# Kernel tuning notes

Measured on AMD Instinct MI355X. Metric: run time of the kernel, lower is better.

## Reference

```python
import jax, jax.numpy as jnp
import numpy as np

D = 1024      # input_dim = clip_model.text_projection.shape[1]
P = D // 8    # pre_dim1 == pre_dim2 == 128
B, NS, NT, C = 4096, 8192, 8192, 1000
EPS = 1e-5
SCALE = 0.1
BETA_S = 1.0
BETA_T = 1.0


def setup_inputs() -> dict:
    key = jax.random.key(0)
    ks = jax.random.split(key, 24)
    rn = lambda k, shp, s=0.02: jax.random.normal(k, shp, dtype=jnp.float32) * s
    inp = {
        "Ft": jax.random.normal(ks[0], (C, D), dtype=jnp.float32),
        "Fv": jax.random.normal(ks[1], (B, D), dtype=jnp.float32),
        "Fvs_bank": jax.random.normal(ks[2], (NS, D), dtype=jnp.float32),
        "Fvt_bank": jax.random.normal(ks[3], (NT, D), dtype=jnp.float32),
        # pre_project: Linear(D->P), BN(P), ReLU, Linear(P->P), BN(P), ReLU, Linear(P->3D)
        "W1": rn(ks[4], (P, D)), "b1": jnp.zeros((P,), jnp.float32),
        "g1": jnp.ones((P,), jnp.float32), "be1": jnp.zeros((P,), jnp.float32),
        "m1": jnp.zeros((P,), jnp.float32), "v1": jnp.ones((P,), jnp.float32),
        "W2": rn(ks[5], (P, P)), "b2": jnp.zeros((P,), jnp.float32),
        "g2": jnp.ones((P,), jnp.float32), "be2": jnp.zeros((P,), jnp.float32),
        "m2": jnp.zeros((P,), jnp.float32), "v2": jnp.ones((P,), jnp.float32),
        "W3": rn(ks[6], (3 * D, P)), "b3": jnp.zeros((3 * D,), jnp.float32),
        # post_project: Linear(D->D)
        "Wp": rn(ks[7], (D, D)), "bp": jnp.zeros((D,), jnp.float32),
        "logit_scale": jnp.asarray(np.log(1.0 / 0.07), dtype=jnp.float32),
    }
    return inp


def _pre_project(x, W1, b1, g1, be1, m1, v1, W2, b2, g2, be2, m2, v2, W3, b3):
    # Linear -> BatchNorm1d (eval: running stats) -> ReLU, twice, then Linear to 3*D
    h = x @ W1.T + b1
    h = jax.nn.relu((h - m1) * jax.lax.rsqrt(v1 + EPS) * g1 + be1)
    h = h @ W2.T + b2
    h = jax.nn.relu((h - m2) * jax.lax.rsqrt(v2 + EPS) * g2 + be2)
    return h @ W3.T + b3  # (n, 3*D)


def _qkv(o):
    # einops 'b (d k) -> k b d' with k=3: interleaved split along last dim
    o = o.reshape(o.shape[0], D, 3)
    return o[..., 0], o[..., 1], o[..., 2]


def reference(Ft, Fv, Fvs_bank, Fvt_bank, W1, b1, g1, be1, m1, v1,
              W2, b2, g2, be2, m2, v2, W3, b3, Wp, bp, logit_scale):
    pre = lambda x: _pre_project(x, W1, b1, g1, be1, m1, v1,
                                 W2, b2, g2, be2, m2, v2, W3, b3)
    q_fv, _, _ = _qkv(pre(Fv))
    _, k_fvs, v_fvs = _qkv(pre(Fvs_bank))
    _, k_fvt, v_fvt = _qkv(pre(Fvt_bank))

    As = jax.nn.softmax(SCALE * (q_fv @ k_fvs.T), axis=-1)  # (B, NS)
    At = jax.nn.softmax(SCALE * (q_fv @ k_fvt.T), axis=-1)  # (B, NT)

    Fsa = Fv + (As @ v_fvs) @ Wp.T + bp
    Fta = Fv + (At @ v_fvt) @ Wp.T + bp
    Fsa = Fsa / jnp.linalg.norm(Fsa, axis=-1, keepdims=True)
    Fta = Fta / jnp.linalg.norm(Fta, axis=-1, keepdims=True)

    ls = jnp.exp(logit_scale)
    logits = BETA_S * ls * (Fsa @ Ft.T) + BETA_T * ls * (Fta @ Ft.T)
    return logits  # (B, C)
```

## Files before the change

kernel.cpp:

```cpp
#include <hip/hip_runtime.h>
#include <hip/hip_bf16.h>
#include <math.h>

#define D_DIM   1024
#define P_DIM   128
#define B_ROWS  4096
#define NBANK   8192
#define C_CLS   1000
#define EPS_BN  1e-5f
#define SCALE_S 0.1f
#define MTOT    20480
#define KVSEG   16
#define KCH     64
#define CHUNKS  (NBANK / KVSEG / KCH)

typedef __bf16 bf16x8 __attribute__((ext_vector_type(8)));
typedef float  f32x4  __attribute__((ext_vector_type(4)));
typedef __hip_bfloat16 bf;

__device__ __forceinline__ void load_lds16(const void* gp, void* lp) {
    __builtin_amdgcn_global_load_lds(
        (__attribute__((address_space(1))) void*)gp,
        (__attribute__((address_space(3))) void*)lp, 16, 0, 0);
}

__device__ __forceinline__ int4 pack8(float4 a, float4 b) {
    union { bf h[8]; int4 v; } u;
    u.h[0] = __float2bfloat16(a.x); u.h[1] = __float2bfloat16(a.y);
    u.h[2] = __float2bfloat16(a.z); u.h[3] = __float2bfloat16(a.w);
    u.h[4] = __float2bfloat16(b.x); u.h[5] = __float2bfloat16(b.y);
    u.h[6] = __float2bfloat16(b.z); u.h[7] = __float2bfloat16(b.w);
    return u.v;
}

__global__ __launch_bounds__(256)
void gemm_bf16(const bf* __restrict__ A, const bf* __restrict__ B,
               const bf* __restrict__ B2,
               int M, int N, int K, int lda, int ldb,
               int kchunks, int fx, int fy, int epi,
               float* __restrict__ Cf, bf* __restrict__ Cb,
               const float* __restrict__ bias, const float* __restrict__ biasm,
               const float* __restrict__ bng, const float* __restrict__ bnb,
               const float* __restrict__ bnm, const float* __restrict__ bnv,
               const float* __restrict__ addsrc, const float* __restrict__ lsp,
               int ldc)
{
    __shared__ __align__(16) short ldsS[8192];
    short* lsA = ldsS;
    short* lsB = ldsS + 4096;

    const int tid  = threadIdx.x;
    const int wave = tid >> 6;
    const int lane = tid & 63;
    const int wm   = wave >> 1;
    const int wn   = wave & 1;
    const int r16  = lane & 15;
    const int quad = lane >> 4;

    int bx, by;
    if (fx == 0) {
        bx = blockIdx.x; by = blockIdx.y;
    } else {
        const int gx = gridDim.x, gy = gridDim.y;
        const int l   = blockIdx.y * gx + blockIdx.x;
        const int xcd = l & 7;
        const int i0  = l >> 3;
        const int sx  = gx / fx, sy = gy / fy;
        bx = (xcd % fx) * sx + (i0 % sx);
        by = (xcd / fx) * sy + (i0 / sx);
    }
    const int bm0 = by * 128;
    const int bn0 = bx * 128;
    const bf* Bp = (B2 && by > 0) ? B2 : B;

    const int kper = K / kchunks;
    const int kbeg = blockIdx.z * kper;
    const int kend = kbeg + kper;

    f32x4 acc[4][4];
#pragma unroll
    for (int i = 0; i < 4; ++i)
#pragma unroll
        for (int j = 0; j < 4; ++j) acc[i][j] = (f32x4){0.f, 0.f, 0.f, 0.f};

    for (int k0 = kbeg; k0 < kend; k0 += 32) {
#pragma unroll
        for (int i = 0; i < 2; ++i) {
            const int s   = i * 256 + tid;
            const int row = s >> 2;
            const int cc  = (s & 3) * 8;
            const int lofs = (i * 256 + wave * 64) * 16;
            load_lds16(A + (size_t)(bm0 + row) * lda + k0 + cc, (char*)lsA + lofs);
            load_lds16(Bp + (size_t)(bn0 + row) * ldb + k0 + cc, (char*)lsB + lofs);
        }
        __syncthreads();

        bf16x8 af[4], bfr[4];
#pragma unroll
        for (int i = 0; i < 4; ++i)
            af[i] = *(const bf16x8*)(lsA + (wm * 64 + i * 16 + r16) * 32 + quad * 8);
#pragma unroll
        for (int j = 0; j < 4; ++j)
            bfr[j] = *(const bf16x8*)(lsB + (wn * 64 + j * 16 + r16) * 32 + quad * 8);
#pragma unroll
        for (int i = 0; i < 4; ++i)
#pragma unroll
            for (int j = 0; j < 4; ++j)
                acc[i][j] = __builtin_amdgcn_mfma_f32_16x16x32_bf16(
                    af[i], bfr[j], acc[i][j], 0, 0, 0);
        __syncthreads();
    }

    if (epi == 8) {
        float* dst = Cf + (size_t)blockIdx.z * M * N;
#pragma unroll
        for (int i = 0; i < 4; ++i) {
            const int gmb = bm0 + wm * 64 + i * 16 + quad * 4;
#pragma unroll
            for (int j = 0; j < 4; ++j) {
                const int gn = bn0 + wn * 64 + j * 16 + r16;
#pragma unroll
                for (int r = 0; r < 4; ++r)
                    dst[(size_t)(gmb + r) * N + gn] = acc[i][j][r];
            }
        }
        return;
    }

    if (epi == 3 || epi == 4) {
        const float lsv = (epi == 4) ? expf(*lsp) : 1.0f;
#pragma unroll
        for (int i = 0; i < 4; ++i) {
            const int gmb = bm0 + wm * 64 + i * 16 + quad * 4;
#pragma unroll
            for (int j = 0; j < 4; ++j) {
                const int gn = bn0 + wn * 64 + j * 16 + r16;
#pragma unroll
                for (int r = 0; r < 4; ++r) {
                    const int gm = gmb + r;
                    float val = acc[i][j][r];
                    if (epi == 3) {
                        Cf[(size_t)gm * N + gn] =
                            val + bias[gn] + addsrc[(size_t)(gm & (ldc - 1)) * N + gn];
                    } else {
                        if (gn < ldc) Cf[(size_t)gm * ldc + gn] = val * lsv;
                    }
                }
            }
        }
        return;
    }

    bf* dst = Cb + (epi == 6 ? (size_t)blockIdx.z * M * N : 0);
    bf* my  = (bf*)(ldsS + wave * 2048);

#pragma unroll
    for (int half = 0; half < 2; ++half) {
#pragma unroll
        for (int i2 = 0; i2 < 2; ++i2) {
            const int i = half * 2 + i2;
            const int gmb = bm0 + wm * 64 + i * 16 + quad * 4;
#pragma unroll
            for (int j = 0; j < 4; ++j) {
                const int gn = bn0 + wn * 64 + j * 16 + r16;
#pragma unroll
                for (int r = 0; r < 4; ++r) {
                    float val = acc[i][j][r];
                    if (epi == 1) {
                        val += bias[gn];
                        val = (val - bnm[gn]) * rsqrtf(bnv[gn] + EPS_BN) * bng[gn] + bnb[gn];
                        val = fmaxf(val, 0.f);
                    } else {
                        if (bias)  val += bias[gn];
                        if (biasm) val += biasm[gmb + r];
                    }
                    my[(i2 * 16 + quad * 4 + r) * 64 + j * 16 + r16] =
                        __float2bfloat16(val);
                }
            }
        }
#pragma unroll
        for (int it = 0; it < 4; ++it) {
            const int chunk = it * 64 + lane;
            const int lrow  = chunk >> 3;
            const int lcol  = (chunk & 7) * 8;
            const int grow  = bm0 + wm * 64 + half * 32 + lrow;
            const int gcol  = bn0 + wn * 64 + lcol;
            int4 v = *(const int4*)(my + lrow * 64 + lcol);
            *(int4*)(dst + (size_t)grow * N + gcol) = v;
        }
    }
}

__global__ __launch_bounds__(256)
void h2fuse(const float* __restrict__ Hp,
            const bf* __restrict__ W2b,
            const bf* __restrict__ Wqk,
            const float* __restrict__ bnA,
            const float* __restrict__ vvecP,
            bf* __restrict__ h2b, bf* __restrict__ qtb,
            float* __restrict__ beta, bf* __restrict__ h2T)
{
    __shared__ __align__(16) short lsH[16384];
    __shared__ __align__(16) short lsW[16384];
    __shared__ float sA1[128], sC1[128], sA2[128], sC2[128];

    const int tid  = threadIdx.x;
    const int wave = tid >> 6;
    const int lane = tid & 63;
    const int r16  = lane & 15;
    const int quad = lane >> 4;
    const int wm   = wave >> 1;
    const int wn   = wave & 1;
    const int r0   = blockIdx.x * 128;
    const bool isq = (r0 < B_ROWS);

#pragma unroll
    for (int m = 0; m < 8; ++m) {
        const int s = m * 256 + tid;
        const int row = s >> 4, pcg = s & 15;
        load_lds16(W2b + row * 128 + (pcg ^ (row & 15)) * 8,
                   (char*)lsW + (m * 256 + wave * 64) * 16);
    }
    if (tid < 128) {
        sA1[tid] = bnA[tid];       sC1[tid] = bnA[128 + tid];
        sA2[tid] = bnA[256 + tid]; sC2[tid] = bnA[384 + tid];
    }
    __syncthreads();

#pragma unroll
    for (int m = 0; m < 16; ++m) {
        const int s = m * 256 + tid;
        const int row = s >> 5;
        const int col = (s & 31) * 4;
        const float* p0 = Hp + (size_t)(r0 + row) * 128 + col;
        float4 x0 = *(const float4*)p0;
        float4 x1 = *(const float4*)(p0 + (size_t)MTOT * 128);
        union { bf h[4]; int2 v; } u;
        u.h[0] = __float2bfloat16(fmaxf(fmaf(x0.x + x1.x, sA1[col],     sC1[col]),     0.f));
        u.h[1] = __float2bfloat16(fmaxf(fmaf(x0.y + x1.y, sA1[col + 1], sC1[col + 1]), 0.f));
        u.h[2] = __float2bfloat16(fmaxf(fmaf(x0.z + x1.z, sA1[col + 2], sC1[col + 2]), 0.f));
        u.h[3] = __float2bfloat16(fmaxf(fmaf(x0.w + x1.w, sA1[col + 3], sC1[col + 3]), 0.f));
        const int cg = col >> 3;
        *(int2*)((bf*)lsH + row * 128 + ((cg ^ (row & 15)) << 3) + (col & 7)) = u.v;
    }
    __syncthreads();

    f32x4 acc[4][4];
#pragma unroll
    for (int i = 0; i < 4; ++i)
#pragma unroll
        for (int j = 0; j < 4; ++j) acc[i][j] = (f32x4){0.f, 0.f, 0.f, 0.f};
#pragma unroll
    for (int ks = 0; ks < 4; ++ks) {
        bf16x8 af[4], bfr[4];
#pragma unroll
        for (int i = 0; i < 4; ++i) {
            const int row = wm * 64 + i * 16 + r16;
            af[i] = *(const bf16x8*)(lsH + row * 128 + ((ks * 4 + quad) ^ (row & 15)) * 8);
        }
#pragma unroll
        for (int j = 0; j < 4; ++j) {
            const int row = wn * 64 + j * 16 + r16;
            bfr[j] = *(const bf16x8*)(lsW + row * 128 + ((ks * 4 + quad) ^ (row & 15)) * 8);
        }
#pragma unroll
        for (int i = 0; i < 4; ++i)
#pragma unroll
            for (int j = 0; j < 4; ++j)
                acc[i][j] = __builtin_amdgcn_mfma_f32_16x16x32_bf16(
                    af[i], bfr[j], acc[i][j], 0, 0, 0);
    }
    __syncthreads();

    if (isq) {
#pragma unroll
        for (int m = 0; m < 8; ++m) {
            const int s = m * 256 + tid;
            const int row = s >> 4, pcg = s & 15;
            load_lds16(Wqk + row * 128 + (pcg ^ (row & 15)) * 8,
                       (char*)lsW + (m * 256 + wave * 64) * 16);
        }
    }

#pragma unroll
    for (int i = 0; i < 4; ++i) {
#pragma unroll
        for (int j = 0; j < 4; ++j) {
            const int gn = wn * 64 + j * 16 + r16;
            const int cg = gn >> 3, cl = gn & 7;
            const float a2 = sA2[gn], c2 = sC2[gn];
#pragma unroll
            for (int r = 0; r < 4; ++r) {
                const int row = wm * 64 + i * 16 + quad * 4 + r;
                float v = fmaxf(fmaf(acc[i][j][r], a2, c2), 0.f);
                ((bf*)lsH)[row * 128 + ((cg ^ (row & 15)) << 3) + cl] =
                    __float2bfloat16(v);
            }
        }
    }
    __syncthreads();

    if (!isq) {
#pragma unroll
        for (int m = 0; m < 8; ++m) {
            const int s = m * 256 + tid;
            const int row = s >> 4, cg = s & 15;
            *(int4*)(h2b + (size_t)(r0 + row) * 128 + cg * 8) =
                *(const int4*)(lsH + row * 128 + ((cg ^ (row & 15)) << 3));
        }
        if (tid < 128) {
            float s = 0.f;
#pragma unroll
            for (int z = 0; z < 16; ++z) s += vvecP[z * 128 + tid];
            sA1[tid] = s;
        }
        __syncthreads();
        const int nb0 = r0 - B_ROWS;
        {
            const int row = tid >> 1, hf = tid & 1;
            float s = 0.f;
#pragma unroll
            for (int g = 0; g < 8; ++g) {
                const int cg = hf * 8 + g;
                bf16x8 v = *(const bf16x8*)(lsH + row * 128 + ((cg ^ (row & 15)) << 3));
#pragma unroll
                for (int e = 0; e < 8; ++e)
                    s += __bfloat162float((bf)v[e]) * sA1[cg * 8 + e];
            }
            s += __shfl_xor(s, 1, 64);
            if (hf == 0) beta[nb0 + row] = s;
        }
#pragma unroll
        for (int m = 0; m < 8; ++m) {
            const int idx = m * 256 + tid;
            const int p  = idx >> 4;
            const int ng = (idx & 15) * 8;
            union { bf h[8]; int4 v; } u;
#pragma unroll
            for (int e = 0; e < 8; ++e) {
                const int n = ng + e;
                u.h[e] = ((bf*)lsH)[n * 128 + (((p >> 3) ^ (n & 15)) << 3) + (p & 7)];
            }
            *(int4*)(h2T + (size_t)p * (2 * NBANK) + nb0 + ng) = u.v;
        }
        return;
    }

    f32x4 acc2[4][4];
#pragma unroll
    for (int i = 0; i < 4; ++i)
#pragma unroll
        for (int j = 0; j < 4; ++j) acc2[i][j] = (f32x4){0.f, 0.f, 0.f, 0.f};
#pragma unroll
    for (int ks = 0; ks < 4; ++ks) {
        bf16x8 af[4], bfr[4];
#pragma unroll
        for (int i = 0; i < 4; ++i) {
            const int row = wm * 64 + i * 16 + r16;
            af[i] = *(const bf16x8*)(lsH + row * 128 + ((ks * 4 + quad) ^ (row & 15)) * 8);
        }
#pragma unroll
        for (int j = 0; j < 4; ++j) {
            const int row = wn * 64 + j * 16 + r16;
            bfr[j] = *(const bf16x8*)(lsW + row * 128 + ((ks * 4 + quad) ^ (row & 15)) * 8);
        }
#pragma unroll
        for (int i = 0; i < 4; ++i)
#pragma unroll
            for (int j = 0; j < 4; ++j)
                acc2[i][j] = __builtin_amdgcn_mfma_f32_16x16x32_bf16(
                    af[i], bfr[j], acc2[i][j], 0, 0, 0);
    }
    __syncthreads();

    bf* my  = (bf*)lsW + wave * 2048;
    bf* dst = qtb + (size_t)r0 * 128;
#pragma unroll
    for (int half = 0; half < 2; ++half) {
#pragma unroll
        for (int i2 = 0; i2 < 2; ++i2) {
            const int i = half * 2 + i2;
#pragma unroll
            for (int j = 0; j < 4; ++j)
#pragma unroll
                for (int r = 0; r < 4; ++r)
                    my[(i2 * 16 + quad * 4 + r) * 64 + j * 16 + r16] =
                        __float2bfloat16(acc2[i][j][r]);
        }
#pragma unroll
        for (int it = 0; it < 4; ++it) {
            const int chunk = it * 64 + lane;
            const int lrow  = chunk >> 3;
            const int lcol  = (chunk & 7) * 8;
            const int grow  = wm * 64 + half * 32 + lrow;
            const int gcol  = wn * 64 + lcol;
            int4 v = *(const int4*)(my + lrow * 64 + lcol);
            *(int4*)(dst + (size_t)grow * 128 + gcol) = v;
        }
    }
}

__global__ __launch_bounds__(512)
void attn_fused(const bf* __restrict__ qt,
                const bf* __restrict__ h2bank,
                const bf* __restrict__ h2T,
                const float* __restrict__ beta,
                bf* __restrict__ Ypart,
                float* __restrict__ rsP)
{
    __shared__ __align__(16) short lds[24576];
    short* lsK = lds;
    short* lsV = lds + 8192;
    short* lsS = lds + 16384;

    const int tid  = threadIdx.x;
    const int wave = tid >> 6;
    const int lane = tid & 63;
    const int r16  = lane & 15;
    const int quad = lane >> 4;

    const int qb   = blockIdx.x >> 5;
    const int side = (blockIdx.x >> 4) & 1;
    const int seg  = blockIdx.x & 15;
    const int part = side * KVSEG + seg;
    const int nseg0 = seg * (NBANK / KVSEG);
    const bf* kbase = h2bank + (size_t)side * NBANK * P_DIM;
    const int ncol0 = side * NBANK;

    const bf* qrow = qt + (size_t)(qb * 128 + wave * 16 + r16) * P_DIM;
    bf16x8 qreg[4];
#pragma unroll
    for (int ks = 0; ks < 4; ++ks)
        qreg[ks] = *(const bf16x8*)(qrow + (ks * 4 + quad) * 8);

    f32x4 yacc[8];
    float rsacc[4] = {0.f, 0.f, 0.f, 0.f};
#pragma unroll
    for (int j = 0; j < 8; ++j) yacc[j] = (f32x4){0.f, 0.f, 0.f, 0.f};

    for (int c = 0; c < CHUNKS; ++c) {
        const int kv0 = nseg0 + c * KCH;
        __syncthreads();
#pragma unroll
        for (int m = 0; m < 2; ++m) {
            const int s = m * 512 + tid;
            const int row = s >> 4, pcg = s & 15;
            const int lcg = pcg ^ (row & 15);
            load_lds16(kbase + (size_t)(kv0 + row) * P_DIM + lcg * 8,
                       (char*)lsK + (m * 512 + wave * 64) * 16);
        }
#pragma unroll
        for (int m = 0; m < 2; ++m) {
            const int s = m * 512 + tid;
            const int row = s >> 3, pcg = s & 7;
            const int lcg = pcg ^ (row & 7);
            load_lds16(h2T + (size_t)row * (2 * NBANK) + ncol0 + kv0 + lcg * 8,
                       (char*)lsV + (m * 512 + wave * 64) * 16);
        }
        __syncthreads();

        f32x4 sacc[4];
#pragma unroll
        for (int j = 0; j < 4; ++j) sacc[j] = (f32x4){0.f, 0.f, 0.f, 0.f};
        __builtin_amdgcn_s_setprio(1);
#pragma unroll
        for (int ks = 0; ks < 4; ++ks) {
            bf16x8 bfr[4];
#pragma unroll
            for (int j = 0; j < 4; ++j) {
                const int kr = j * 16 + r16;
                bfr[j] = *(const bf16x8*)(lsK + kr * 128 +
                                          ((ks * 4 + quad) ^ (kr & 15)) * 8);
            }
#pragma unroll
            for (int j = 0; j < 4; ++j)
                sacc[j] = __builtin_amdgcn_mfma_f32_16x16x32_bf16(
                    qreg[ks], bfr[j], sacc[j], 0, 0, 0);
        }
        __builtin_amdgcn_s_setprio(0);

#pragma unroll
        for (int j = 0; j < 4; ++j) {
            const int col = j * 16 + r16;
            const float bv = beta[(size_t)side * NBANK + kv0 + col];
            const int cg = col >> 3, cl = col & 7;
#pragma unroll
            for (int r = 0; r < 4; ++r) {
                const int row = wave * 16 + quad * 4 + r;
                float v = __expf(SCALE_S * (sacc[j][r] + bv));
                rsacc[r] += v;
                ((bf*)lsS)[row * 64 + ((cg ^ (row & 7)) << 3) + cl] =
                    __float2bfloat16(v);
            }
        }

        __builtin_amdgcn_s_setprio(1);
#pragma unroll
        for (int ks = 0; ks < 2; ++ks) {
            const int sr = wave * 16 + r16;
            bf16x8 pa = *(const bf16x8*)(lsS + sr * 64 +
                                         ((ks * 4 + quad) ^ (sr & 7)) * 8);
            bf16x8 pb[8];
#pragma unroll
            for (int j = 0; j < 8; ++j) {
                const int vr = j * 16 + r16;
                pb[j] = *(const bf16x8*)(lsV + vr * 64 +
                                         ((ks * 4 + quad) ^ (vr & 7)) * 8);
            }
#pragma unroll
            for (int j = 0; j < 8; ++j)
                yacc[j] = __builtin_amdgcn_mfma_f32_16x16x32_bf16(
                    pa, pb[j], yacc[j], 0, 0, 0);
        }
        __builtin_amdgcn_s_setprio(0);
    }

#pragma unroll
    for (int r = 0; r < 4; ++r) {
        float s = rsacc[r];
        s += __shfl_xor(s, 1, 64);
        s += __shfl_xor(s, 2, 64);
        s += __shfl_xor(s, 4, 64);
        s += __shfl_xor(s, 8, 64);
        rsacc[r] = s;
    }
    if (r16 == 0)
        *(float4*)(rsP + (size_t)part * B_ROWS + qb * 128 + wave * 16 + quad * 4) =
            (float4){rsacc[0], rsacc[1], rsacc[2], rsacc[3]};

    __syncthreads();
    bf* my = (bf*)lds + wave * 2048;
#pragma unroll
    for (int j = 0; j < 8; ++j)
#pragma unroll
        for (int r = 0; r < 4; ++r)
            my[(quad * 4 + r) * 128 + j * 16 + r16] =
                __float2bfloat16(yacc[j][r]);
    bf* dst = Ypart + (size_t)part * B_ROWS * P_DIM
                    + (size_t)(qb * 128 + wave * 16) * P_DIM;
#pragma unroll
    for (int it = 0; it < 4; ++it) {
        const int chunk = it * 64 + lane;
        const int lrow  = chunk >> 4;
        const int lcol  = (chunk & 15) * 8;
        *(int4*)(dst + (size_t)lrow * P_DIM + lcol) =
            *(const int4*)(my + lrow * 128 + lcol);
    }
}

#define PG0 10240
#define PG1 584
#define PG2 64
#define PG3 512
#define PG4 8
#define PG5 256
#define PG6 1

__global__ __launch_bounds__(256)
void prep(const float* __restrict__ Fv, const float* __restrict__ Fvs,
          const float* __restrict__ Fvt,
          const float* __restrict__ W1, const float* __restrict__ W2,
          const float* __restrict__ Wp,
          const float* __restrict__ W3, const float* __restrict__ b3,
          const float* __restrict__ bp, const float* __restrict__ Ft,
          const float* __restrict__ b1, const float* __restrict__ g1,
          const float* __restrict__ be1, const float* __restrict__ m1,
          const float* __restrict__ v1,
          const float* __restrict__ b2, const float* __restrict__ g2,
          const float* __restrict__ be2, const float* __restrict__ m2,
          const float* __restrict__ v2,
          bf* __restrict__ Xb, bf* __restrict__ W1b, bf* __restrict__ W2b,
          bf* __restrict__ Wpb,
          bf* __restrict__ Tq, bf* __restrict__ Tk, bf* __restrict__ Tv,
          bf* __restrict__ Ftb,
          float* __restrict__ vvecP, float* __restrict__ bvp,
          float* __restrict__ bnA)
{
    const int tid = threadIdx.x;
    int b = blockIdx.x;
    if (b < PG0) {
        int i = (b * 256 + tid) * 8;
        const int n0 = B_ROWS * D_DIM, n1 = n0 + NBANK * D_DIM;
        const float* src; int off;
        if (i < n0)      { src = Fv;  off = i; }
        else if (i < n1) { src = Fvs; off = i - n0; }
        else             { src = Fvt; off = i - n1; }
        float4 a = *(const float4*)(src + off);
        float4 c = *(const float4*)(src + off + 4);
        *(int4*)(Xb + i) = pack8(a, c);
        return;
    }
    if ((b -= PG0) < PG1) {
        int i = (b * 256 + tid) * 8;
        const int n1 = P_DIM * D_DIM, n2 = n1 + P_DIM * P_DIM;
        const float* src; bf* dst; int off;
        if (i < n1)      { src = W1; dst = W1b; off = i; }
        else if (i < n2) { src = W2; dst = W2b; off = i - n1; }
        else             { src = Wp; dst = Wpb; off = i - n2; }
        float4 a = *(const float4*)(src + off);
        float4 c = *(const float4*)(src + off + 4);
        *(int4*)(dst + off) = pack8(a, c);
        return;
    }
    if ((b -= PG1) < PG2) {
        int i = (b * 256 + tid) * 8;
        int p = i >> 10, d0 = i & 1023;
        union { bf h[8]; int4 v; } uq, uk, uv;
#pragma unroll
        for (int j = 0; j < 8; ++j) {
            const float* r = W3 + (size_t)3 * (d0 + j) * P_DIM + p;
            uq.h[j] = __float2bfloat16(r[0]);
            uk.h[j] = __float2bfloat16(r[P_DIM]);
            uv.h[j] = __float2bfloat16(r[2 * P_DIM]);
        }
        *(int4*)(Tq + i) = uq.v;
        *(int4*)(Tk + i) = uk.v;
        *(int4*)(Tv + i) = uv.v;
        return;
    }
    if ((b -= PG2) < PG3) {
        int i = (b * 256 + tid) * 8;
        int row = i >> 10, col = i & 1023;
        if (row < C_CLS) {
            float4 a = *(const float4*)(Ft + (size_t)row * D_DIM + col);
            float4 c = *(const float4*)(Ft + (size_t)row * D_DIM + col + 4);
            *(int4*)(Ftb + i) = pack8(a, c);
        } else {
            *(int4*)(Ftb + i) = (int4){0, 0, 0, 0};
        }
        return;
    }
    if ((b -= PG3) < PG4) {
        const int p = tid & 127, hf = tid >> 7;
        const int dbase = b * 128 + hf * 64;
        float s = 0.f;
        for (int dd = 0; dd < 64; ++dd) {
            const int d = dbase + dd;
            s = fmaf(b3[3 * d], W3[(size_t)(3 * d + 1) * P_DIM + p], s);
        }
        vvecP[(b * 2 + hf) * P_DIM + p] = s;
        return;
    }
    if ((b -= PG4) < PG5) {
        const int wave = tid >> 6, lane = tid & 63;
        const int o = b * 4 + wave;
        const float* r = Wp + (size_t)o * D_DIM;
        float s = 0.f;
        for (int i = lane; i < D_DIM; i += 64) s = fmaf(r[i], b3[3 * i + 2], s);
        for (int off = 32; off > 0; off >>= 1) s += __shfl_down(s, off, 64);
        if (lane == 0) bvp[o] = s + bp[o];
        return;
    }
    if (tid < 128) {
        float a1 = g1[tid] * rsqrtf(v1[tid] + EPS_BN);
        bnA[tid]       = a1;
        bnA[128 + tid] = (b1[tid] - m1[tid]) * a1 + be1[tid];
        float a2 = g2[tid] * rsqrtf(v2[tid] + EPS_BN);
        bnA[256 + tid] = a2;
        bnA[384 + tid] = (b2[tid] - m2[tid]) * a2 + be2[tid];
    }
}

__global__ __launch_bounds__(256)
void reduceWW(const bf* __restrict__ WWp,
              bf* __restrict__ Wqk, bf* __restrict__ Wpv)
{
    const int tid = threadIdx.x;
    const size_t pstride = (size_t)1152 * 128;
    if (blockIdx.x < 8) {
        int i = (blockIdx.x * 256 + tid) * 8;
        float s[8] = {};
        for (int z = 0; z < 8; ++z) {
            union { int4 v; bf h[8]; } u;
            u.v = *(const int4*)(WWp + (size_t)z * pstride + i);
#pragma unroll
            for (int e = 0; e < 8; ++e) s[e] += __bfloat162float(u.h[e]);
        }
        union { bf h[8]; int4 v; } o;
#pragma unroll
        for (int e = 0; e < 8; ++e) o.h[e] = __float2bfloat16(s[e]);
        *(int4*)(Wqk + i) = o.v;
    } else {
        int i = ((blockIdx.x - 8) * 256 + tid) * 8;
        float s[8] = {};
        for (int z = 0; z < 8; ++z) {
            union { int4 v; bf h[8]; } u;
            u.v = *(const int4*)(WWp + (size_t)z * pstride + 16384 + i);
#pragma unroll
            for (int e = 0; e < 8; ++e) s[e] += __bfloat162float(u.h[e]);
        }
        union { bf h[8]; int4 v; } o;
#pragma unroll
        for (int e = 0; e < 8; ++e) o.h[e] = __float2bfloat16(s[e]);
        *(int4*)(Wpv + i) = o.v;
    }
}

__global__ __launch_bounds__(256)
void reduceY(const bf* __restrict__ parts, const float* __restrict__ rsP,
             bf* __restrict__ Yhat)
{
    int j = (blockIdx.x * 256 + threadIdx.x) * 8;
    const int s = j >> 19;
    const int qrow = (j >> 7) & (B_ROWS - 1);
    float rs = 0.f;
#pragma unroll
    for (int g = 0; g < KVSEG; ++g)
        rs += rsP[(size_t)(s * KVSEG + g) * B_ROWS + qrow];
    const bf* p = parts + (size_t)s * KVSEG * 524288 + (size_t)(j & 524287);
    float acc[8] = {};
    for (int z = 0; z < KVSEG; ++z) {
        union { int4 v; bf h[8]; } u;
        u.v = *(const int4*)(p + (size_t)z * 524288);
#pragma unroll
        for (int e = 0; e < 8; ++e) acc[e] += __bfloat162float(u.h[e]);
    }
    const float inv = 1.0f / rs;
    union { bf h[8]; int4 v; } o;
#pragma unroll
    for (int e = 0; e < 8; ++e) o.h[e] = __float2bfloat16(acc[e] * inv);
    *(int4*)(Yhat + j) = o.v;
}

__global__ __launch_bounds__(256)
void rownorm2b(const float* __restrict__ G, bf* __restrict__ out)
{
    __shared__ float red[16];
    const int tid = threadIdx.x;
    const float* ps = G + (size_t)blockIdx.x * D_DIM;
    const float* pt = ps + (size_t)B_ROWS * D_DIM;
    float4 a = *(const float4*)(ps + tid * 4);
    float4 c = *(const float4*)(pt + tid * 4);
    float sa = a.x * a.x + a.y * a.y + a.z * a.z + a.w * a.w;
    float sb = c.x * c.x + c.y * c.y + c.z * c.z + c.w * c.w;
    for (int s = 32; s > 0; s >>= 1) {
        sa += __shfl_down(sa, s, 64);
        sb += __shfl_down(sb, s, 64);
    }
    if ((tid & 63) == 0) { red[tid >> 6] = sa; red[8 + (tid >> 6)] = sb; }
    __syncthreads();
    if (tid == 0) {
        float ta = 0.f, tb = 0.f;
        for (int w = 0; w < 4; ++w) { ta += red[w]; tb += red[8 + w]; }
        red[4] = rsqrtf(ta); red[12] = rsqrtf(tb);
    }
    __syncthreads();
    const float ia = red[4], ib = red[12];
    union { bf h[4]; int2 v; } o;
    o.h[0] = __float2bfloat16(a.x * ia + c.x * ib);
    o.h[1] = __float2bfloat16(a.y * ia + c.y * ib);
    o.h[2] = __float2bfloat16(a.z * ia + c.z * ib);
    o.h[3] = __float2bfloat16(a.w * ia + c.w * ib);
    *(int2*)(out + (size_t)blockIdx.x * D_DIM + tid * 4) = o.v;
}

extern "C" void kernel_launch(void* const* d_in, const int* in_sizes, int n_in,
                              void* d_out, int out_size, void* d_ws, size_t ws_size,
                              hipStream_t stream)
{
    (void)in_sizes; (void)n_in; (void)out_size; (void)ws_size;

    const float* Ft  = (const float*)d_in[0];
    const float* Fv  = (const float*)d_in[1];
    const float* Fvs = (const float*)d_in[2];
    const float* Fvt = (const float*)d_in[3];
    const float* W1  = (const float*)d_in[4];
    const float* b1  = (const float*)d_in[5];
    const float* g1  = (const float*)d_in[6];
    const float* be1 = (const float*)d_in[7];
    const float* m1  = (const float*)d_in[8];
    const float* v1  = (const float*)d_in[9];
    const float* W2  = (const float*)d_in[10];
    const float* b2  = (const float*)d_in[11];
    const float* g2  = (const float*)d_in[12];
    const float* be2 = (const float*)d_in[13];
    const float* m2  = (const float*)d_in[14];
    const float* v2  = (const float*)d_in[15];
    const float* W3  = (const float*)d_in[16];
    const float* b3  = (const float*)d_in[17];
    const float* Wp  = (const float*)d_in[18];
    const float* bp  = (const float*)d_in[19];
    const float* ls  = (const float*)d_in[20];

    char* base = (char*)d_ws;
    size_t o = 0;
    auto take = [&](size_t s) { size_t r = o; o += (s + 255) & ~(size_t)255; return r; };

    bf* qtb   = (bf*)(base + take((size_t)B_ROWS * P_DIM * 2));
    bf* h2T   = (bf*)(base + take((size_t)P_DIM * 2 * NBANK * 2));
    bf* Yhat  = (bf*)(base + take((size_t)2 * B_ROWS * P_DIM * 2));
    bf* Ftb   = (bf*)(base + take((size_t)D_DIM * D_DIM * 2));
    bf* W3qT  = (bf*)(base + take((size_t)P_DIM * D_DIM * 2));
    bf* W3kT  = (bf*)(base + take((size_t)P_DIM * D_DIM * 2));
    bf* Wpb   = (bf*)(base + take((size_t)D_DIM * D_DIM * 2));
    bf* W3vT  = (bf*)(base + take((size_t)P_DIM * D_DIM * 2));
    bf* Wqk   = (bf*)(base + take((size_t)P_DIM * P_DIM * 2));
    bf* Wpvb  = (bf*)(base + take((size_t)D_DIM * P_DIM * 2));
    bf* W1b   = (bf*)(base + take((size_t)P_DIM * D_DIM * 2));
    bf* W2b   = (bf*)(base + take((size_t)P_DIM * P_DIM * 2));
    bf* h2b   = (bf*)(base + take((size_t)MTOT * P_DIM * 2));
    bf* WWp   = (bf*)(base + take((size_t)8 * 1152 * P_DIM * 2));
    float* vvecP = (float*)(base + take((size_t)16 * P_DIM * 4));
    float* beta  = (float*)(base + take((size_t)2 * NBANK * 4));
    float* bvp   = (float*)(base + take(D_DIM * 4));
    float* bnA   = (float*)(base + take(4 * P_DIM * 4));
    float* rsP   = (float*)(base + take((size_t)2 * KVSEG * B_ROWS * 4));

    const size_t Dbase = o;
    bf*    Xb    = (bf*)(base + Dbase);
    float* Hp    = (float*)(base + Dbase + (size_t)MTOT * D_DIM * 2);
    bf*    Opart = (bf*)(base + Dbase + (size_t)64 * 1024 * 1024);
    float* G     = (float*)(base + Dbase);
    bf*    Fsumb = (bf*)(base + Dbase + (size_t)2 * B_ROWS * D_DIM * 4);

    auto gemm = [&](const bf* A, const bf* B, const bf* B2,
                    int M, int N, int K, int lda, int ldb,
                    int kch, int fx, int fy, int epi, float* Cf, bf* Cb,
                    const float* bias, const float* biasm,
                    const float* bg, const float* bb, const float* bm, const float* bv,
                    const float* addsrc, const float* lsp, int ldc) {
        gemm_bf16<<<dim3(N / 128, M / 128, kch), dim3(256), 0, stream>>>(
            A, B, B2, M, N, K, lda, ldb, kch, fx, fy, epi, Cf, Cb, bias, biasm,
            bg, bb, bm, bv, addsrc, lsp, ldc);
    };

    prep<<<dim3(PG0 + PG1 + PG2 + PG3 + PG4 + PG5 + PG6), dim3(256), 0, stream>>>(
        Fv, Fvs, Fvt, W1, W2, Wp, W3, b3, bp, Ft,
        b1, g1, be1, m1, v1, b2, g2, be2, m2, v2,
        Xb, W1b, W2b, Wpb, W3qT, W3kT, W3vT, Ftb, vvecP, bvp, bnA);

    gemm(W3kT, W3qT, W3vT, 1152, P_DIM, D_DIM, D_DIM, D_DIM, 8, 0, 0, 6,
         nullptr, WWp, nullptr, nullptr, nullptr, nullptr, nullptr, nullptr,
         nullptr, nullptr, 0);
    reduceWW<<<dim3(72), dim3(256), 0, stream>>>(WWp, Wqk, Wpvb);

    gemm(Xb, W1b, nullptr, MTOT, P_DIM, D_DIM, D_DIM, D_DIM, 2, 1, 8, 8,
         Hp, nullptr, nullptr, nullptr, nullptr, nullptr, nullptr, nullptr,
         nullptr, nullptr, 0);
    h2fuse<<<dim3(MTOT / 128), dim3(256), 0, stream>>>(
        Hp, W2b, Wqk, bnA, vvecP, h2b, qtb, beta, h2T);

    attn_fused<<<dim3(2 * KVSEG * (B_ROWS / 128)), dim3(512), 0, stream>>>(
        qtb, h2b + (size_t)B_ROWS * P_DIM, h2T, beta, Opart, rsP);
    reduceY<<<dim3(2 * B_ROWS * P_DIM / 2048), dim3(256), 0, stream>>>(
        Opart, rsP, Yhat);

    gemm(Yhat, Wpvb, nullptr, 2 * B_ROWS, D_DIM, P_DIM, P_DIM, P_DIM, 1, 1, 8, 3,
         G, nullptr, bvp, nullptr, nullptr, nullptr, nullptr, nullptr, Fv,
         nullptr, B_ROWS);
    rownorm2b<<<dim3(B_ROWS), dim3(256), 0, stream>>>(G, Fsumb);
    gemm(Fsumb, Ftb, nullptr, B_ROWS, D_DIM, D_DIM, D_DIM, D_DIM, 1, 1, 8, 4,
         (float*)d_out, nullptr, nullptr, nullptr, nullptr, nullptr, nullptr,
         nullptr, nullptr, ls, C_CLS);
}
```

Baseline: 328.4 us.

## Fuse fp32-to-bf16 input conversion into first GEMM and double-buffer attention KV

The separate prep pass that converted Fv and both banks to bf16 is removed. The first projection GEMM now reads the fp32 rows directly, packs them to bf16 in registers and stores them to LDS, which avoids writing and re-reading a 20480x1024 bf16 staging buffer. Separately, attn_fused gets double-buffered K/V LDS tiles so the next chunk loads while the current one computes, at the cost of more LDS per block and possibly lower occupancy. The fused A load path uses synchronous global loads instead of async LDS loads, which may stall the GEMM's main loop.

New measurement: 326.9 us. No clear change (-0.4%).

```diff
diff --git a/kernel.cpp b/kernel.cpp
--- a/kernel.cpp
+++ b/kernel.cpp
@@ -36,6 +36,8 @@
 __global__ __launch_bounds__(256)
 void gemm_bf16(const bf* __restrict__ A, const bf* __restrict__ B,
                const bf* __restrict__ B2,
+               const float* __restrict__ Af0, const float* __restrict__ Af1,
+               const float* __restrict__ Af2,
                int M, int N, int K, int lda, int ldb,
                int kchunks, int fx, int fy, int epi,
                float* __restrict__ Cf, bf* __restrict__ Cb,
@@ -73,6 +75,14 @@
     const int bn0 = bx * 128;
     const bf* Bp = (B2 && by > 0) ? B2 : B;
 
+    const float* af = nullptr;
+    int arow0 = 0;
+    if (Af0) {
+        if (bm0 < B_ROWS)              { af = Af0; arow0 = bm0; }
+        else if (bm0 < B_ROWS + NBANK) { af = Af1; arow0 = bm0 - B_ROWS; }
+        else                           { af = Af2; arow0 = bm0 - B_ROWS - NBANK; }
+    }
+
     const int kper = K / kchunks;
     const int kbeg = blockIdx.z * kper;
     const int kend = kbeg + kper;
@@ -90,15 +100,23 @@
             const int row = s >> 2;
             const int cc  = (s & 3) * 8;
             const int lofs = (i * 256 + wave * 64) * 16;
-            load_lds16(A + (size_t)(bm0 + row) * lda + k0 + cc, (char*)lsA + lofs);
+            if (af) {
+                const float* p = af + (size_t)(arow0 + row) * lda + k0 + cc;
+                float4 a = *(const float4*)p;
+                float4 b = *(const float4*)(p + 4);
+                *(int4*)((char*)lsA + s * 16) = pack8(a, b);
+            } else {
+                load_lds16(A + (size_t)(bm0 + row) * lda + k0 + cc,
+                           (char*)lsA + lofs);
+            }
             load_lds16(Bp + (size_t)(bn0 + row) * ldb + k0 + cc, (char*)lsB + lofs);
         }
         __syncthreads();
 
-        bf16x8 af[4], bfr[4];
+        bf16x8 afr[4], bfr[4];
 #pragma unroll
         for (int i = 0; i < 4; ++i)
-            af[i] = *(const bf16x8*)(lsA + (wm * 64 + i * 16 + r16) * 32 + quad * 8);
+            afr[i] = *(const bf16x8*)(lsA + (wm * 64 + i * 16 + r16) * 32 + quad * 8);
 #pragma unroll
         for (int j = 0; j < 4; ++j)
             bfr[j] = *(const bf16x8*)(lsB + (wn * 64 + j * 16 + r16) * 32 + quad * 8);
@@ -107,7 +125,7 @@
 #pragma unroll
             for (int j = 0; j < 4; ++j)
                 acc[i][j] = __builtin_amdgcn_mfma_f32_16x16x32_bf16(
-                    af[i], bfr[j], acc[i][j], 0, 0, 0);
+                    afr[i], bfr[j], acc[i][j], 0, 0, 0);
         __syncthreads();
     }
 
@@ -409,10 +427,8 @@
                 bf* __restrict__ Ypart,
                 float* __restrict__ rsP)
 {
-    __shared__ __align__(16) short lds[24576];
-    short* lsK = lds;
-    short* lsV = lds + 8192;
-    short* lsS = lds + 16384;
+    __shared__ __align__(16) short lds[40960];
+    short* lsS = lds + 32768;
 
     const int tid  = threadIdx.x;
     const int wave = tid >> 6;
@@ -439,16 +455,16 @@
 #pragma unroll
     for (int j = 0; j < 8; ++j) yacc[j] = (f32x4){0.f, 0.f, 0.f, 0.f};
 
-    for (int c = 0; c < CHUNKS; ++c) {
-        const int kv0 = nseg0 + c * KCH;
-        __syncthreads();
+    auto stage = [&](int buf, int kv0) {
+        short* dK = lds + buf * 8192;
+        short* dV = lds + 16384 + buf * 8192;
 #pragma unroll
         for (int m = 0; m < 2; ++m) {
             const int s = m * 512 + tid;
             const int row = s >> 4, pcg = s & 15;
             const int lcg = pcg ^ (row & 15);
             load_lds16(kbase + (size_t)(kv0 + row) * P_DIM + lcg * 8,
-                       (char*)lsK + (m * 512 + wave * 64) * 16);
+                       (char*)dK + (m * 512 + wave * 64) * 16);
         }
 #pragma unroll
         for (int m = 0; m < 2; ++m) {
@@ -456,9 +472,20 @@
             const int row = s >> 3, pcg = s & 7;
             const int lcg = pcg ^ (row & 7);
             load_lds16(h2T + (size_t)row * (2 * NBANK) + ncol0 + kv0 + lcg * 8,
-                       (char*)lsV + (m * 512 + wave * 64) * 16);
-        }
+                       (char*)dV + (m * 512 + wave * 64) * 16);
+        }
+    };
+
+    stage(0, nseg0);
+    int cur = 0;
+
+    for (int c = 0; c < CHUNKS; ++c) {
         __syncthreads();
+        if (c + 1 < CHUNKS) stage(cur ^ 1, nseg0 + (c + 1) * KCH);
+
+        short* lsK = lds + cur * 8192;
+        short* lsV = lds + 16384 + cur * 8192;
+        const int kv0 = nseg0 + c * KCH;
 
         f32x4 sacc[4];
 #pragma unroll
@@ -514,6 +541,7 @@
                     pa, pb[j], yacc[j], 0, 0, 0);
         }
         __builtin_amdgcn_s_setprio(0);
+        cur ^= 1;
     }
 
 #pragma unroll
@@ -549,18 +577,15 @@
     }
 }
 
-#define PG0 10240
-#define PG1 584
-#define PG2 64
-#define PG3 512
-#define PG4 8
-#define PG5 256
-#define PG6 1
+#define PG0 584
+#define PG1 64
+#define PG2 512
+#define PG3 8
+#define PG4 256
+#define PG5 1
 
 __global__ __launch_bounds__(256)
-void prep(const float* __restrict__ Fv, const float* __restrict__ Fvs,
-          const float* __restrict__ Fvt,
-          const float* __restrict__ W1, const float* __restrict__ W2,
+void prep(const float* __restrict__ W1, const float* __restrict__ W2,
           const float* __restrict__ Wp,
           const float* __restrict__ W3, const float* __restrict__ b3,
           const float* __restrict__ bp, const float* __restrict__ Ft,
@@ -570,8 +595,7 @@
           const float* __restrict__ b2, const float* __restrict__ g2,
           const float* __restrict__ be2, const float* __restrict__ m2,
           const float* __restrict__ v2,
-          bf* __restrict__ Xb, bf* __restrict__ W1b, bf* __restrict__ W2b,
-          bf* __restrict__ Wpb,
+          bf* __restrict__ W1b, bf* __restrict__ W2b, bf* __restrict__ Wpb,
           bf* __restrict__ Tq, bf* __restrict__ Tk, bf* __restrict__ Tv,
           bf* __restrict__ Ftb,
           float* __restrict__ vvecP, float* __restrict__ bvp,
@@ -580,18 +604,6 @@
     const int tid = threadIdx.x;
     int b = blockIdx.x;
     if (b < PG0) {
-        int i = (b * 256 + tid) * 8;
-        const int n0 = B_ROWS * D_DIM, n1 = n0 + NBANK * D_DIM;
-        const float* src; int off;
-        if (i < n0)      { src = Fv;  off = i; }
-        else if (i < n1) { src = Fvs; off = i - n0; }
-        else             { src = Fvt; off = i - n1; }
-        float4 a = *(const float4*)(src + off);
-        float4 c = *(const float4*)(src + off + 4);
-        *(int4*)(Xb + i) = pack8(a, c);
-        return;
-    }
-    if ((b -= PG0) < PG1) {
         int i = (b * 256 + tid) * 8;
         const int n1 = P_DIM * D_DIM, n2 = n1 + P_DIM * P_DIM;
         const float* src; bf* dst; int off;
@@ -603,7 +615,7 @@
         *(int4*)(dst + off) = pack8(a, c);
         return;
     }
-    if ((b -= PG1) < PG2) {
+    if ((b -= PG0) < PG1) {
         int i = (b * 256 + tid) * 8;
         int p = i >> 10, d0 = i & 1023;
         union { bf h[8]; int4 v; } uq, uk, uv;
@@ -619,7 +631,7 @@
         *(int4*)(Tv + i) = uv.v;
         return;
     }
-    if ((b -= PG2) < PG3) {
+    if ((b -= PG1) < PG2) {
         int i = (b * 256 + tid) * 8;
         int row = i >> 10, col = i & 1023;
         if (row < C_CLS) {
@@ -631,7 +643,7 @@
         }
         return;
     }
-    if ((b -= PG3) < PG4) {
+    if ((b -= PG2) < PG3) {
         const int p = tid & 127, hf = tid >> 7;
         const int dbase = b * 128 + hf * 64;
         float s = 0.f;
@@ -642,7 +654,7 @@
         vvecP[(b * 2 + hf) * P_DIM + p] = s;
         return;
     }
-    if ((b -= PG4) < PG5) {
+    if ((b -= PG3) < PG4) {
         const int wave = tid >> 6, lane = tid & 63;
         const int o = b * 4 + wave;
         const float* r = Wp + (size_t)o * D_DIM;
@@ -808,34 +820,36 @@
     float* rsP   = (float*)(base + take((size_t)2 * KVSEG * B_ROWS * 4));
 
     const size_t Dbase = o;
-    bf*    Xb    = (bf*)(base + Dbase);
-    float* Hp    = (float*)(base + Dbase + (size_t)MTOT * D_DIM * 2);
+    float* Hp    = (float*)(base + Dbase);
     bf*    Opart = (bf*)(base + Dbase + (size_t)64 * 1024 * 1024);
     float* G     = (float*)(base + Dbase);
     bf*    Fsumb = (bf*)(base + Dbase + (size_t)2 * B_ROWS * D_DIM * 4);
 
     auto gemm = [&](const bf* A, const bf* B, const bf* B2,
+                    const float* Af0, const float* Af1, const float* Af2,
                     int M, int N, int K, int lda, int ldb,
                     int kch, int fx, int fy, int epi, float* Cf, bf* Cb,
                     const float* bias, const float* biasm,
                     const float* bg, const float* bb, const float* bm, const float* bv,
                     const float* addsrc, const float* lsp, int ldc) {
         gemm_bf16<<<dim3(N / 128, M / 128, kch), dim3(256), 0, stream>>>(
-            A, B, B2, M, N, K, lda, ldb, kch, fx, fy, epi, Cf, Cb, bias, biasm,
-            bg, bb, bm, bv, addsrc, lsp, ldc);
+            A, B, B2, Af0, Af1, Af2, M, N, K, lda, ldb, kch, fx, fy, epi,
+            Cf, Cb, bias, biasm, bg, bb, bm, bv, addsrc, lsp, ldc);
     };
 
-    prep<<<dim3(PG0 + PG1 + PG2 + PG3 + PG4 + PG5 + PG6), dim3(256), 0, stream>>>(
-        Fv, Fvs, Fvt, W1, W2, Wp, W3, b3, bp, Ft,
+    prep<<<dim3(PG0 + PG1 + PG2 + PG3 + PG4 + PG5), dim3(256), 0, stream>>>(
+        W1, W2, Wp, W3, b3, bp, Ft,
         b1, g1, be1, m1, v1, b2, g2, be2, m2, v2,
-        Xb, W1b, W2b, Wpb, W3qT, W3kT, W3vT, Ftb, vvecP, bvp, bnA);
-
-    gemm(W3kT, W3qT, W3vT, 1152, P_DIM, D_DIM, D_DIM, D_DIM, 8, 0, 0, 6,
+        W1b, W2b, Wpb, W3qT, W3kT, W3vT, Ftb, vvecP, bvp, bnA);
+
+    gemm(W3kT, W3qT, W3vT, nullptr, nullptr, nullptr,
+         1152, P_DIM, D_DIM, D_DIM, D_DIM, 8, 0, 0, 6,
          nullptr, WWp, nullptr, nullptr, nullptr, nullptr, nullptr, nullptr,
          nullptr, nullptr, 0);
     reduceWW<<<dim3(72), dim3(256), 0, stream>>>(WWp, Wqk, Wpvb);
 
-    gemm(Xb, W1b, nullptr, MTOT, P_DIM, D_DIM, D_DIM, D_DIM, 2, 1, 8, 8,
+    gemm(nullptr, W1b, nullptr, Fv, Fvs, Fvt,
+         MTOT, P_DIM, D_DIM, D_DIM, D_DIM, 2, 1, 8, 8,
          Hp, nullptr, nullptr, nullptr, nullptr, nullptr, nullptr, nullptr,
          nullptr, nullptr, 0);
     h2fuse<<<dim3(MTOT / 128), dim3(256), 0, stream>>>(
@@ -846,11 +860,13 @@
     reduceY<<<dim3(2 * B_ROWS * P_DIM / 2048), dim3(256), 0, stream>>>(
         Opart, rsP, Yhat);
 
-    gemm(Yhat, Wpvb, nullptr, 2 * B_ROWS, D_DIM, P_DIM, P_DIM, P_DIM, 1, 1, 8, 3,
+    gemm(Yhat, Wpvb, nullptr, nullptr, nullptr, nullptr,
+         2 * B_ROWS, D_DIM, P_DIM, P_DIM, P_DIM, 1, 1, 8, 3,
          G, nullptr, bvp, nullptr, nullptr, nullptr, nullptr, nullptr, Fv,
          nullptr, B_ROWS);
     rownorm2b<<<dim3(B_ROWS), dim3(256), 0, stream>>>(G, Fsumb);
-    gemm(Fsumb, Ftb, nullptr, B_ROWS, D_DIM, D_DIM, D_DIM, D_DIM, 1, 1, 8, 4,
+    gemm(Fsumb, Ftb, nullptr, nullptr, nullptr, nullptr,
+         B_ROWS, D_DIM, D_DIM, D_DIM, D_DIM, 1, 1, 8, 4,
          (float*)d_out, nullptr, nullptr, nullptr, nullptr, nullptr, nullptr,
          nullptr, nullptr, ls, C_CLS);
 }
```
